# Performance work log

Hardware: AMD Instinct MI355X
Metric: run time of the kernel (lower is better)

The kernel has to match this reference:

```python
import jax, jax.numpy as jnp
import numpy as np

EMBED_DIM = 768
NUM_HEADS = 12
HEAD_DIM = EMBED_DIM // NUM_HEADS


def setup_inputs() -> dict:
    key = jax.random.key(0)
    k1, k2, k3, k4 = jax.random.split(key, 4)
    B, N, E = 8, 1024, EMBED_DIM
    x = jax.random.normal(k1, (B, N, E), dtype=jnp.float32)
    # qkv: Linear(E, 3E, bias=False); proj: Linear(E, E) with bias
    w_qkv = jax.random.normal(k2, (E, 3 * E), dtype=jnp.float32) * (1.0 / np.sqrt(E))
    w_proj = jax.random.normal(k3, (E, E), dtype=jnp.float32) * (1.0 / np.sqrt(E))
    b_proj = jax.random.normal(k4, (E,), dtype=jnp.float32) * 0.01
    return {"x": x, "w_qkv": w_qkv, "w_proj": w_proj, "b_proj": b_proj}


def reference(x, w_qkv, w_proj, b_proj):
    B, N, E = x.shape
    H, D = NUM_HEADS, HEAD_DIM
    scale = D ** -0.5
    # qkv projection: [B, N, 3E] -> [3, B, H, N, D]
    qkv = (x @ w_qkv).reshape(B, N, 3, H, D).transpose(2, 0, 3, 1, 4)
    q, k, v = qkv[0], qkv[1], qkv[2]
    # attention scores [B, H, N, N], explicitly materialized (returned)
    attn = jax.nn.softmax(jnp.einsum('bhnd,bhmd->bhnm', q, k) * scale, axis=-1)
    # dropout is identity in eval mode
    out = jnp.einsum('bhnm,bhmd->bhnd', attn, v)  # [B, H, N, D]
    out = out.transpose(0, 2, 1, 3).reshape(B, N, E)  # [B, N, E]
    out = out @ w_proj + b_proj
    return (out, attn)
```

## Files before the change

kernel.cpp:

```cpp
#include <hip/hip_runtime.h>
#include <hip/hip_fp16.h>


typedef _Float16 f16x8 __attribute__((ext_vector_type(8)));
typedef _Float16 f16x4 __attribute__((ext_vector_type(4)));
typedef float f32x4 __attribute__((ext_vector_type(4)));

#define B_ 8
#define N_ 1024
#define E_ 768
#define H_ 12
#define D_ 64

__global__ __launch_bounds__(256) void cast_x_kernel(const float* __restrict__ in,
                                                     _Float16* __restrict__ out, int n4) {
  int stride = gridDim.x * blockDim.x;
  for (int i = blockIdx.x * blockDim.x + threadIdx.x; i < n4; i += stride) {
    float4 v = reinterpret_cast<const float4*>(in)[i];
    f16x4 o = { (_Float16)v.x, (_Float16)v.y, (_Float16)v.z, (_Float16)v.w };
    reinterpret_cast<f16x4*>(out)[i] = o;
  }
}

__global__ __launch_bounds__(256) void transpose_cast_kernel(const float* __restrict__ in,
                                                             _Float16* __restrict__ out,
                                                             int rows, int cols) {
  __shared__ float tile[32][33];
  int c0 = blockIdx.x * 32, r0 = blockIdx.y * 32;
  int tx = threadIdx.x & 31, ty = threadIdx.x >> 5;
  #pragma unroll
  for (int i = 0; i < 32; i += 8)
    tile[ty + i][tx] = in[(size_t)(r0 + ty + i) * cols + c0 + tx];
  __syncthreads();
  #pragma unroll
  for (int i = 0; i < 32; i += 8)
    out[(size_t)(c0 + ty + i) * rows + r0 + tx] = (_Float16)tile[tx][ty + i];
}

__global__ __launch_bounds__(256) void gemm_qkv_kernel(const _Float16* __restrict__ A,
                                                       const _Float16* __restrict__ Bt,
                                                       _Float16* __restrict__ q,
                                                       _Float16* __restrict__ k,
                                                       _Float16* __restrict__ vt) {
  __shared__ _Float16 As[128 * 32];
  __shared__ _Float16 Bs[128 * 32];
  const int tid = threadIdx.x, lane = tid & 63, w = tid >> 6;
  const int wr = w >> 1, wc = w & 1;
  const int m0 = blockIdx.y * 128, n0 = blockIdx.x * 128;
  const f32x4 zero = {0.f, 0.f, 0.f, 0.f};
  f32x4 acc[4][4];
  #pragma unroll
  for (int m = 0; m < 4; m++)
    #pragma unroll
    for (int n = 0; n < 4; n++) acc[m][n] = zero;
  const int srow = lane >> 2;
  const int skof = (lane & 3) * 8;
  for (int k0 = 0; k0 < 768; k0 += 32) {
    #pragma unroll
    for (int i = 0; i < 2; i++) {
      int c = w * 2 + i;
      int row = c * 16 + srow;
      const _Float16* ga = A + (size_t)(m0 + row) * 768 + k0 + skof;
      __builtin_amdgcn_global_load_lds((const __attribute__((address_space(1))) void*)ga,
                                       (__attribute__((address_space(3))) void*)(As + c * 512),
                                       16, 0, 0);
      const _Float16* gb = Bt + (size_t)(n0 + row) * 768 + k0 + skof;
      __builtin_amdgcn_global_load_lds((const __attribute__((address_space(1))) void*)gb,
                                       (__attribute__((address_space(3))) void*)(Bs + c * 512),
                                       16, 0, 0);
    }
    __syncthreads();
    f16x8 af[4], bfr[4];
    #pragma unroll
    for (int m = 0; m < 4; m++)
      af[m] = *reinterpret_cast<const f16x8*>(&As[(wr * 64 + m * 16 + (lane & 15)) * 32 + (lane >> 4) * 8]);
    #pragma unroll
    for (int n = 0; n < 4; n++)
      bfr[n] = *reinterpret_cast<const f16x8*>(&Bs[(wc * 64 + n * 16 + (lane & 15)) * 32 + (lane >> 4) * 8]);
    #pragma unroll
    for (int m = 0; m < 4; m++)
      #pragma unroll
      for (int n = 0; n < 4; n++)
        acc[m][n] = __builtin_amdgcn_mfma_f32_16x16x32_f16(af[m], bfr[n], acc[m][n], 0, 0, 0);
    __syncthreads();
  }
  const int g = lane >> 4, cc = lane & 15;
  #pragma unroll
  for (int n = 0; n < 4; n++) {
    int C = n0 + wc * 64 + n * 16 + cc;
    int mat = C / 768;
    int e = C - mat * 768;
    int h = e >> 6, d = e & 63;
    #pragma unroll
    for (int m = 0; m < 4; m++) {
      int R0 = m0 + wr * 64 + m * 16 + 4 * g;
      int b = R0 >> 10, nn0 = R0 & 1023;
      if (mat == 2) {
        f16x4 pk = { (_Float16)acc[m][n][0], (_Float16)acc[m][n][1],
                     (_Float16)acc[m][n][2], (_Float16)acc[m][n][3] };
        *reinterpret_cast<f16x4*>(&vt[(((size_t)b * H_ + h) * D_ + d) * N_ + nn0]) = pk;
      } else {
        _Float16* dst = (mat == 0) ? q : k;
        #pragma unroll
        for (int j = 0; j < 4; j++)
          dst[(((size_t)b * H_ + h) * N_ + nn0 + j) * D_ + d] = (_Float16)acc[m][n][j];
      }
    }
  }
}

__global__ __launch_bounds__(512, 4) void attn_kernel(const _Float16* __restrict__ Q,
                                                      const _Float16* __restrict__ K,
                                                      const _Float16* __restrict__ Vt,
                                                      float* __restrict__ attn_out,
                                                      _Float16* __restrict__ pv) {
  __shared__ __align__(16) _Float16 S[32 * 1024];
  const int bh = blockIdx.y;
  const int qbase = blockIdx.x * 32;
  const int tid = threadIdx.x, lane = tid & 63, w = tid >> 6;
  const int g = lane >> 4, cc = lane & 15;
  const _Float16* Qp = Q + ((size_t)bh * N_ + qbase) * D_;
  const _Float16* Kp = K + (size_t)bh * N_ * D_;
  const _Float16* Vp = Vt + (size_t)bh * D_ * N_;
  const float scale = 0.125f;
  const f32x4 zero = {0.f, 0.f, 0.f, 0.f};

  f16x8 aq[2][2];
  #pragma unroll
  for (int rt = 0; rt < 2; rt++)
    #pragma unroll
    for (int ks = 0; ks < 2; ks++)
      aq[rt][ks] = *reinterpret_cast<const f16x8*>(Qp + (size_t)(rt * 16 + cc) * D_ + ks * 32 + g * 8);
  for (int ct = w; ct < 64; ct += 8) {
    f16x8 kb[2];
    #pragma unroll
    for (int ks = 0; ks < 2; ks++)
      kb[ks] = *reinterpret_cast<const f16x8*>(Kp + (size_t)(ct * 16 + cc) * D_ + ks * 32 + g * 8);
    #pragma unroll
    for (int rt = 0; rt < 2; rt++) {
      f32x4 s = zero;
      s = __builtin_amdgcn_mfma_f32_16x16x32_f16(aq[rt][0], kb[0], s, 0, 0, 0);
      s = __builtin_amdgcn_mfma_f32_16x16x32_f16(aq[rt][1], kb[1], s, 0, 0, 0);
      #pragma unroll
      for (int j = 0; j < 4; j++)
        S[(rt * 16 + 4 * g + j) * 1024 + ct * 16 + cc] = (_Float16)(s[j] * scale);
    }
  }
  __syncthreads();

  const int r = w * 4 + g;
  f16x8 sreg[8];
  float mx = -3.0e38f;
  #pragma unroll
  for (int i = 0; i < 8; i++) {
    sreg[i] = *reinterpret_cast<const f16x8*>(&S[r * 1024 + cc * 8 + 128 * i]);
    #pragma unroll
    for (int j = 0; j < 8; j++) mx = fmaxf(mx, (float)sreg[i][j]);
  }
  #pragma unroll
  for (int m = 1; m < 16; m <<= 1) mx = fmaxf(mx, __shfl_xor(mx, m));
  float sum = 0.f;
  #pragma unroll
  for (int i = 0; i < 8; i++) {
    #pragma unroll
    for (int j = 0; j < 8; j++) {
      float p = __expf((float)sreg[i][j] - mx);
      sum += p;
      sreg[i][j] = (_Float16)p;
    }
  }
  #pragma unroll
  for (int m = 1; m < 16; m <<= 1) sum += __shfl_xor(sum, m);
  const float iv = 1.f / sum;

  float* Ao = attn_out + ((size_t)bh * N_ + qbase + r) * N_;
  #pragma unroll
  for (int i = 0; i < 8; i++) {
    float pn[8];
    #pragma unroll
    for (int j = 0; j < 8; j++) {
      pn[j] = (float)sreg[i][j] * iv;
      sreg[i][j] = (_Float16)pn[j];
    }
    float4 o0 = {pn[0], pn[1], pn[2], pn[3]};
    float4 o1 = {pn[4], pn[5], pn[6], pn[7]};
    reinterpret_cast<float4*>(Ao + cc * 8 + 128 * i)[0] = o0;
    reinterpret_cast<float4*>(Ao + cc * 8 + 128 * i + 4)[0] = o1;
  }
  __syncthreads();

  #pragma unroll
  for (int i = 0; i < 8; i++) {
    int kc = cc + 16 * i;
    int blk = kc * 32 + (r ^ ((2 * kc) & 31));
    *reinterpret_cast<f16x8*>(&S[blk * 8]) = sreg[i];
  }
  __syncthreads();

  const int rt = w >> 2, dt = w & 3;
  const _Float16* vrow = Vp + (size_t)(dt * 16 + cc) * N_;
  f32x4 acc = zero;
  #pragma unroll 2
  for (int k0 = 0; k0 < N_; k0 += 32) {
    int kc = (k0 >> 3) + g;
    int blk = kc * 32 + ((rt * 16 + cc) ^ ((2 * kc) & 31));
    f16x8 pa = *reinterpret_cast<const f16x8*>(&S[blk * 8]);
    f16x8 vb = *reinterpret_cast<const f16x8*>(vrow + k0 + g * 8);
    acc = __builtin_amdgcn_mfma_f32_16x16x32_f16(pa, vb, acc, 0, 0, 0);
  }
  const int b = bh / H_, h = bh - b * H_;
  #pragma unroll
  for (int j = 0; j < 4; j++) {
    int n = qbase + rt * 16 + 4 * g + j;
    pv[((size_t)b * N_ + n) * E_ + h * 64 + dt * 16 + cc] = (_Float16)acc[j];
  }
}

__global__ __launch_bounds__(256) void gemm_proj_kernel(const _Float16* __restrict__ A,
                                                        const _Float16* __restrict__ Bt,
                                                        const float* __restrict__ bias,
                                                        float* __restrict__ out) {
  __shared__ _Float16 As[128 * 32];
  __shared__ _Float16 Bs[128 * 32];
  const int tid = threadIdx.x, lane = tid & 63, w = tid >> 6;
  const int wr = w >> 1, wc = w & 1;
  const int m0 = blockIdx.y * 128, n0 = blockIdx.x * 128;
  const f32x4 zero = {0.f, 0.f, 0.f, 0.f};
  f32x4 acc[4][4];
  #pragma unroll
  for (int m = 0; m < 4; m++)
    #pragma unroll
    for (int n = 0; n < 4; n++) acc[m][n] = zero;
  const int srow = lane >> 2;
  const int skof = (lane & 3) * 8;
  for (int k0 = 0; k0 < 768; k0 += 32) {
    #pragma unroll
    for (int i = 0; i < 2; i++) {
      int c = w * 2 + i;
      int row = c * 16 + srow;
      const _Float16* ga = A + (size_t)(m0 + row) * 768 + k0 + skof;
      __builtin_amdgcn_global_load_lds((const __attribute__((address_space(1))) void*)ga,
                                       (__attribute__((address_space(3))) void*)(As + c * 512),
                                       16, 0, 0);
      const _Float16* gb = Bt + (size_t)(n0 + row) * 768 + k0 + skof;
      __builtin_amdgcn_global_load_lds((const __attribute__((address_space(1))) void*)gb,
                                       (__attribute__((address_space(3))) void*)(Bs + c * 512),
                                       16, 0, 0);
    }
    __syncthreads();
    f16x8 af[4], bfr[4];
    #pragma unroll
    for (int m = 0; m < 4; m++)
      af[m] = *reinterpret_cast<const f16x8*>(&As[(wr * 64 + m * 16 + (lane & 15)) * 32 + (lane >> 4) * 8]);
    #pragma unroll
    for (int n = 0; n < 4; n++)
      bfr[n] = *reinterpret_cast<const f16x8*>(&Bs[(wc * 64 + n * 16 + (lane & 15)) * 32 + (lane >> 4) * 8]);
    #pragma unroll
    for (int m = 0; m < 4; m++)
      #pragma unroll
      for (int n = 0; n < 4; n++)
        acc[m][n] = __builtin_amdgcn_mfma_f32_16x16x32_f16(af[m], bfr[n], acc[m][n], 0, 0, 0);
    __syncthreads();
  }
  const int g = lane >> 4, cc = lane & 15;
  #pragma unroll
  for (int n = 0; n < 4; n++) {
    int C = n0 + wc * 64 + n * 16 + cc;
    float bb = bias[C];
    #pragma unroll
    for (int m = 0; m < 4; m++) {
      #pragma unroll
      for (int j = 0; j < 4; j++) {
        int R = m0 + wr * 64 + m * 16 + 4 * g + j;
        out[(size_t)R * 768 + C] = acc[m][n][j] + bb;
      }
    }
  }
}

extern "C" void kernel_launch(void* const* d_in, const int* in_sizes, int n_in,
                              void* d_out, int out_size, void* d_ws, size_t ws_size,
                              hipStream_t stream) {
  const float* x      = (const float*)d_in[0];
  const float* w_qkv  = (const float*)d_in[1];
  const float* w_proj = (const float*)d_in[2];
  const float* b_proj = (const float*)d_in[3];
  float* out  = (float*)d_out;
  float* attn = out + (size_t)B_ * N_ * E_;

  char* ws = (char*)d_ws;
  const size_t SZ_XH    = (size_t)B_ * N_ * E_ * 2;
  const size_t SZ_WQKVT = (size_t)E_ * 3 * E_ * 2;
  const size_t SZ_WPROJT= (size_t)E_ * E_ * 2;
  _Float16* xh     = (_Float16*)(ws);
  _Float16* wqkvT  = (_Float16*)(ws + SZ_XH);
  _Float16* wprojT = (_Float16*)(ws + SZ_XH + SZ_WQKVT);
  _Float16* qh     = (_Float16*)(ws + SZ_XH + SZ_WQKVT + SZ_WPROJT);
  _Float16* kh     = qh + (size_t)B_ * H_ * N_ * D_;
  _Float16* vth    = kh + (size_t)B_ * H_ * N_ * D_;
  _Float16* pvh    = vth + (size_t)B_ * H_ * N_ * D_;

  cast_x_kernel<<<dim3(2048), dim3(256), 0, stream>>>(x, xh, (B_ * N_ * E_) / 4);
  transpose_cast_kernel<<<dim3(3 * E_ / 32, E_ / 32), dim3(256), 0, stream>>>(w_qkv, wqkvT, E_, 3 * E_);
  transpose_cast_kernel<<<dim3(E_ / 32, E_ / 32), dim3(256), 0, stream>>>(w_proj, wprojT, E_, E_);
  gemm_qkv_kernel<<<dim3(3 * E_ / 128, B_ * N_ / 128), dim3(256), 0, stream>>>(xh, wqkvT, qh, kh, vth);
  attn_kernel<<<dim3(N_ / 32, B_ * H_), dim3(512), 0, stream>>>(qh, kh, vth, attn, pvh);
  gemm_proj_kernel<<<dim3(E_ / 128, B_ * N_ / 128), dim3(256), 0, stream>>>(pvh, wprojT, b_proj, out);
}
```

Baseline: 650.0 us.

## Prefetch K/V fragments, swizzle score LDS writes, use nontemporal stores for outputs

Software-prefetches the next K tile in the score loop and the next V fragment in the PV loop so global loads overlap the MFMA work. Score writes to shared memory are XOR-swizzled by lane group to cut bank conflicts, and the softmax read, attention write and P re-store follow the same permuted column mapping. Attention and projection outputs are written with nontemporal stores to avoid polluting the cache. This raises register pressure and makes the column-index bookkeeping more involved.

```diff
diff --git a/kernel.cpp b/kernel.cpp
--- a/kernel.cpp
+++ b/kernel.cpp
@@ -131,24 +131,30 @@
     #pragma unroll
     for (int ks = 0; ks < 2; ks++)
       aq[rt][ks] = *reinterpret_cast<const f16x8*>(Qp + (size_t)(rt * 16 + cc) * D_ + ks * 32 + g * 8);
+  f16x8 kb0 = *reinterpret_cast<const f16x8*>(Kp + (size_t)(w * 16 + cc) * D_ + g * 8);
+  f16x8 kb1 = *reinterpret_cast<const f16x8*>(Kp + (size_t)(w * 16 + cc) * D_ + 32 + g * 8);
   for (int ct = w; ct < 64; ct += 8) {
-    f16x8 kb[2];
-    #pragma unroll
-    for (int ks = 0; ks < 2; ks++)
-      kb[ks] = *reinterpret_cast<const f16x8*>(Kp + (size_t)(ct * 16 + cc) * D_ + ks * 32 + g * 8);
+    int ctn = (ct + 8 < 64) ? ct + 8 : w;
+    f16x8 nb0 = *reinterpret_cast<const f16x8*>(Kp + (size_t)(ctn * 16 + cc) * D_ + g * 8);
+    f16x8 nb1 = *reinterpret_cast<const f16x8*>(Kp + (size_t)(ctn * 16 + cc) * D_ + 32 + g * 8);
     #pragma unroll
     for (int rt = 0; rt < 2; rt++) {
       f32x4 s = zero;
-      s = __builtin_amdgcn_mfma_f32_16x16x32_f16(aq[rt][0], kb[0], s, 0, 0, 0);
-      s = __builtin_amdgcn_mfma_f32_16x16x32_f16(aq[rt][1], kb[1], s, 0, 0, 0);
+      s = __builtin_amdgcn_mfma_f32_16x16x32_f16(aq[rt][0], kb0, s, 0, 0, 0);
+      s = __builtin_amdgcn_mfma_f32_16x16x32_f16(aq[rt][1], kb1, s, 0, 0, 0);
       #pragma unroll
-      for (int j = 0; j < 4; j++)
-        S[(rt * 16 + 4 * g + j) * 1024 + ct * 16 + cc] = (_Float16)(s[j] * scale);
-    }
+      for (int j = 0; j < 4; j++) {
+        int row = rt * 16 + 4 * g + j;
+        int col = (ct * 16 + cc) ^ (g << 4);
+        S[row * 1024 + col] = (_Float16)(s[j] * scale);
+      }
+    }
+    kb0 = nb0; kb1 = nb1;
   }
   __syncthreads();
 
   const int r = w * 4 + g;
+  const int rsw = (w & 3) << 4;
   f16x8 sreg[8];
   float mx = -3.0e38f;
   #pragma unroll
@@ -176,22 +182,25 @@
   float* Ao = attn_out + ((size_t)bh * N_ + qbase + r) * N_;
   #pragma unroll
   for (int i = 0; i < 8; i++) {
-    float pn[8];
-    #pragma unroll
-    for (int j = 0; j < 8; j++) {
-      pn[j] = (float)sreg[i][j] * iv;
-      sreg[i][j] = (_Float16)pn[j];
-    }
-    float4 o0 = {pn[0], pn[1], pn[2], pn[3]};
-    float4 o1 = {pn[4], pn[5], pn[6], pn[7]};
-    reinterpret_cast<float4*>(Ao + cc * 8 + 128 * i)[0] = o0;
-    reinterpret_cast<float4*>(Ao + cc * 8 + 128 * i + 4)[0] = o1;
+    int colbase = (cc * 8 + 128 * i) ^ rsw;
+    f32x4 o0, o1;
+    #pragma unroll
+    for (int j = 0; j < 4; j++) {
+      o0[j] = (float)sreg[i][j] * iv;
+      o1[j] = (float)sreg[i][4 + j] * iv;
+    }
+    __builtin_nontemporal_store(o0, reinterpret_cast<f32x4*>(Ao + colbase));
+    __builtin_nontemporal_store(o1, reinterpret_cast<f32x4*>(Ao + colbase + 4));
+    f16x8 pk;
+    #pragma unroll
+    for (int j = 0; j < 4; j++) { pk[j] = (_Float16)o0[j]; pk[4 + j] = (_Float16)o1[j]; }
+    sreg[i] = pk;
   }
   __syncthreads();
 
   #pragma unroll
   for (int i = 0; i < 8; i++) {
-    int kc = cc + 16 * i;
+    int kc = ((cc * 8 + 128 * i) ^ rsw) >> 3;
     int blk = kc * 32 + (r ^ ((2 * kc) & 31));
     *reinterpret_cast<f16x8*>(&S[blk * 8]) = sreg[i];
   }
@@ -200,13 +209,16 @@
   const int rt = w >> 2, dt = w & 3;
   const _Float16* vrow = Vp + (size_t)(dt * 16 + cc) * N_;
   f32x4 acc = zero;
-  #pragma unroll 2
+  f16x8 vb = *reinterpret_cast<const f16x8*>(vrow + g * 8);
+  #pragma unroll 4
   for (int k0 = 0; k0 < N_; k0 += 32) {
+    int kn = (k0 + 32 < N_) ? k0 + 32 : 0;
+    f16x8 vn = *reinterpret_cast<const f16x8*>(vrow + kn + g * 8);
     int kc = (k0 >> 3) + g;
     int blk = kc * 32 + ((rt * 16 + cc) ^ ((2 * kc) & 31));
     f16x8 pa = *reinterpret_cast<const f16x8*>(&S[blk * 8]);
-    f16x8 vb = *reinterpret_cast<const f16x8*>(vrow + k0 + g * 8);
     acc = __builtin_amdgcn_mfma_f32_16x16x32_f16(pa, vb, acc, 0, 0, 0);
+    vb = vn;
   }
   const int b = bh / H_, h = bh - b * H_;
   #pragma unroll
@@ -272,7 +284,7 @@
       #pragma unroll
       for (int j = 0; j < 4; j++) {
         int R = m0 + wr * 64 + m * 16 + 4 * g + j;
-        out[(size_t)R * 768 + C] = acc[m][n][j] + bb;
+        __builtin_nontemporal_store(acc[m][n][j] + bb, &out[(size_t)R * 768 + C]);
       }
     }
   }
```

After: 650.4 us. No clear change (+0.1%).
